# Optimization experiments

Hardware: AMD Instinct MI355X
Metric: run time of the kernel (lower is better)

Reference implementation:

```python
import jax, jax.numpy as jnp
import numpy as np

N, E, EMB, HID, H = 50000, 800000, 128, 512, 8
D = EMB // H
EPS = 1e-5


def _linear_params(key, fan_in, fan_out):
    s = 1.0 / np.sqrt(fan_in)
    k1, k2 = jax.random.split(key)
    w = jax.random.uniform(k1, (fan_in, fan_out), minval=-s, maxval=s, dtype=jnp.float32)
    b = jax.random.uniform(k2, (fan_out,), minval=-s, maxval=s, dtype=jnp.float32)
    return w, b


def setup_inputs() -> dict:
    key = jax.random.key(0)
    ks = jax.random.split(key, 9)
    x = jax.random.normal(ks[0], (N, EMB), dtype=jnp.float32)
    edge_index = jax.random.randint(ks[1], (2, E), 0, N, dtype=jnp.int32)
    batch = jnp.zeros((N,), dtype=jnp.int32)
    wq, bq = _linear_params(ks[2], EMB, EMB)
    wk, bk = _linear_params(ks[3], EMB, EMB)
    wv, bv = _linear_params(ks[4], EMB, EMB)
    wo, bo = _linear_params(ks[5], EMB, EMB)
    w1, b1 = _linear_params(ks[6], EMB, HID)
    w2, b2 = _linear_params(ks[7], HID, EMB)
    g1 = jnp.ones((EMB,), jnp.float32); be1 = jnp.zeros((EMB,), jnp.float32)
    g2 = jnp.ones((EMB,), jnp.float32); be2 = jnp.zeros((EMB,), jnp.float32)
    return {"x": x, "wq": wq, "bq": bq, "wk": wk, "bk": bk, "wv": wv, "bv": bv,
            "wo": wo, "bo": bo, "w1": w1, "b1": b1, "w2": w2, "b2": b2,
            "g1": g1, "be1": be1, "g2": g2, "be2": be2,
            "edge_index": edge_index, "batch": batch, "latent": 0}


def _batchnorm(x, g, b):
    mu = x.mean(axis=0)
    var = ((x - mu) ** 2).mean(axis=0)  # biased, as BatchNorm1d in training
    return g * (x - mu) * jax.lax.rsqrt(var + EPS) + b


def _forward(x, wq, bq, wk, bk, wv, bv, wo, bo, w1, b1, w2, b2, g1, be1, g2, be2, A, B):
    n = x.shape[0]
    q = (x @ wq + bq).reshape(n, H, D)
    k = (x @ wk + bk).reshape(n, H, D)
    v = (x @ wv + bv).reshape(n, H, D)
    # per-edge head-mixing scores: q[A] @ k[B]^T -> [E, H, H]
    score = jnp.einsum('ehd,egd->ehg', q[A], k[B])
    ssum = jax.ops.segment_sum(score, A, num_segments=n)
    cnt = jax.ops.segment_sum(jnp.ones((A.shape[0],), score.dtype), A, num_segments=n)
    score = ssum / jnp.maximum(cnt, 1.0)[:, None, None]  # scatter-mean per node [N,H,H]
    score = jax.nn.softmax(score, axis=-1)
    out = jnp.einsum('ehg,egd->ehd', score, v).reshape(n, EMB)
    out = out @ wo + bo
    x = _batchnorm(out + x, g1, be1)
    h = jax.nn.gelu(x @ w1 + b1, approximate=False)
    h = h @ w2 + b2
    x = _batchnorm(h + x, g2, be2)
    return x


def reference(x, wq, bq, wk, bk, wv, bv, wo, bo, w1, b1, w2, b2, g1, be1, g2, be2, edge_index, batch, latent):
    A, B = edge_index[0], edge_index[1]
    return _forward(x, wq, bq, wk, bk, wv, bv, wo, bo, w1, b1, w2, b2, g1, be1, g2, be2, A, B)
```

## Files before the change

### kernel.cpp

```cpp
#include <hip/hip_runtime.h>
#include <hip/hip_bf16.h>

typedef float f4 __attribute__((ext_vector_type(4)));
typedef short bh8 __attribute__((ext_vector_type(8)));

#define EMB 128
#define HID 512

__device__ __forceinline__ float bfbits2f(unsigned int lo16) {
    unsigned int u = lo16 << 16;
    return __builtin_bit_cast(float, u);
}
__device__ __forceinline__ short f2bf(float f) {
    __hip_bfloat16 h = __float2bfloat16(f);
    return __builtin_bit_cast(short, h);
}

__global__ void hist_kernel(const int* __restrict__ edge, unsigned* __restrict__ cnt, int E) {
    int stride = gridDim.x * blockDim.x;
    for (int e = blockIdx.x * blockDim.x + threadIdx.x; e < E; e += stride)
        atomicAdd(&cnt[edge[e]], 1u);
}

__global__ void scan_blocks(const unsigned* __restrict__ cnt, int* __restrict__ off,
                            int* __restrict__ bsum, int n) {
    __shared__ int ls[256];
    int tid = threadIdx.x;
    int base = blockIdx.x * 1024 + tid * 4;
    int v0 = 0, v1 = 0, v2 = 0, v3 = 0;
    if (base + 0 < n) v0 = (int)cnt[base + 0];
    if (base + 1 < n) v1 = (int)cnt[base + 1];
    if (base + 2 < n) v2 = (int)cnt[base + 2];
    if (base + 3 < n) v3 = (int)cnt[base + 3];
    int s = v0 + v1 + v2 + v3;
    ls[tid] = s;
    __syncthreads();
    for (int d = 1; d < 256; d <<= 1) {
        int t = (tid >= d) ? ls[tid - d] : 0;
        __syncthreads();
        ls[tid] += t;
        __syncthreads();
    }
    int incl = ls[tid];
    int run = incl - s;
    if (tid == 255) bsum[blockIdx.x] = incl;
    if (base + 0 < n) { off[base + 0] = run; run += v0; }
    if (base + 1 < n) { off[base + 1] = run; run += v1; }
    if (base + 2 < n) { off[base + 2] = run; run += v2; }
    if (base + 3 < n) { off[base + 3] = run; }
}

__global__ void scan_bsums(int* __restrict__ bsum, int nb) {
    int lane = threadIdx.x & 63;
    int x = (lane < nb) ? bsum[lane] : 0;
    int orig = x;
#pragma unroll
    for (int o = 1; o < 64; o <<= 1) {
        int t = __shfl_up(x, o, 64);
        if (lane >= o) x += t;
    }
    if (lane < nb) bsum[lane] = x - orig;
}

__global__ void scan_apply(const unsigned* __restrict__ cnt, const int* __restrict__ bsum,
                           int* __restrict__ off, int* __restrict__ offw,
                           float* __restrict__ cntf, int n) {
    int base = blockIdx.x * 1024 + threadIdx.x * 4;
    int add = bsum[blockIdx.x];
#pragma unroll
    for (int i = 0; i < 4; ++i) {
        int idx = base + i;
        if (idx < n) {
            int o = off[idx] + add;
            off[idx] = o;
            offw[idx] = o;
            cntf[idx] = (float)cnt[idx];
        }
    }
}

__global__ void place_kernel(const int* __restrict__ edge, int* __restrict__ offw,
                             int* __restrict__ sortedB, int E) {
    int stride = gridDim.x * blockDim.x;
    for (int e = blockIdx.x * blockDim.x + threadIdx.x; e < E; e += stride) {
        int a = edge[e];
        int pos = atomicAdd(&offw[a], 1);
        sortedB[pos] = edge[E + e];
    }
}

__global__ void prep_all(const float* __restrict__ wq, const float* __restrict__ wk,
                         const float* __restrict__ wv, const float* __restrict__ wo,
                         const float* __restrict__ w1, const float* __restrict__ w2,
                         const float* __restrict__ bq, const float* __restrict__ bk,
                         const float* __restrict__ bv,
                         short* __restrict__ wqkvT, short* __restrict__ woT,
                         short* __restrict__ w1T, short* __restrict__ w2T,
                         float* __restrict__ bqkv) {
    int id = blockIdx.x * blockDim.x + threadIdx.x;
    if (id < 16384) {
        int k = id >> 7, c = id & 127;
        wqkvT[c * 128 + k] = f2bf(wq[id]);
    } else if (id < 32768) {
        int t = id - 16384; int k = t >> 7, c = t & 127;
        wqkvT[(128 + c) * 128 + k] = f2bf(wk[t]);
    } else if (id < 49152) {
        int t = id - 32768; int k = t >> 7, c = t & 127;
        wqkvT[(256 + c) * 128 + k] = f2bf(wv[t]);
    } else if (id < 65536) {
        int t = id - 49152; int k = t >> 7, c = t & 127;
        woT[c * 128 + k] = f2bf(wo[t]);
    } else if (id < 131072) {
        int t = id - 65536; int k = t >> 9, c = t & 511;
        w1T[c * 128 + k] = f2bf(w1[t]);
    } else if (id < 196608) {
        int t = id - 131072; int k = t >> 7, c = t & 127;
        w2T[c * 512 + k] = f2bf(w2[t]);
    }
    if (id < 128) {
        bqkv[id] = bq[id];
        bqkv[128 + id] = bk[id];
        bqkv[256 + id] = bv[id];
    }
}

template<int KT, bool IN_BF16>
__device__ __forceinline__ void ld_ab(bh8 (&av)[4], bh8 (&bv)[4],
                                      const float* __restrict__ Xf, const short* __restrict__ Xb,
                                      const int (&rowA)[4], const short* __restrict__ Wt,
                                      int C0, int l15, int kbase) {
#pragma unroll
    for (int rf = 0; rf < 4; ++rf) {
        if constexpr (IN_BF16) {
            av[rf] = *(const bh8*)(Xb + (size_t)rowA[rf] * KT + kbase);
        } else {
            f4 lo = *(const f4*)(Xf + (size_t)rowA[rf] * KT + kbase);
            f4 hi = *(const f4*)(Xf + (size_t)rowA[rf] * KT + kbase + 4);
            bh8 t;
            t[0] = f2bf(lo[0]); t[1] = f2bf(lo[1]); t[2] = f2bf(lo[2]); t[3] = f2bf(lo[3]);
            t[4] = f2bf(hi[0]); t[5] = f2bf(hi[1]); t[6] = f2bf(hi[2]); t[7] = f2bf(hi[3]);
            av[rf] = t;
        }
    }
#pragma unroll
    for (int cf = 0; cf < 4; ++cf)
        bv[cf] = *(const bh8*)(Wt + (size_t)(C0 + cf * 16 + l15) * KT + kbase);
}

__device__ __forceinline__ void mm16(f4 (&acc)[4][4], const bh8 (&av)[4], const bh8 (&bv)[4]) {
#pragma unroll
    for (int rf = 0; rf < 4; ++rf)
#pragma unroll
        for (int cf = 0; cf < 4; ++cf)
            acc[rf][cf] = __builtin_amdgcn_mfma_f32_16x16x32_bf16(av[rf], bv[cf], acc[rf][cf], 0, 0, 0);
}

#define CSTRIDE 136

template<int KT, bool IN_BF16, bool GELU, bool OUT_BF16, bool RESID, bool RBF16, bool STATS>
__global__ __launch_bounds__(256, 2) void mfma_gemm(
    const void* __restrict__ Xv, const short* __restrict__ Wt, const float* __restrict__ bias,
    const void* __restrict__ resid,
    void* __restrict__ outv, float* __restrict__ slots, int n, int OC, int ncolb, int nrb)
{
    int bx, by;
    if (ncolb == 1) {
        bx = blockIdx.x; by = 0;
    } else {
        int q = blockIdx.x >> 3;
        by = q % ncolb;
        bx = (q / ncolb) * 8 + (blockIdx.x & 7);
        if (bx >= nrb) return;
    }
    const int lane = threadIdx.x & 63;
    const int w = threadIdx.x >> 6;
    const int wr = w >> 1, wc = w & 1;
    const int R0 = bx * 128 + wr * 64;
    const int C0 = by * 128 + wc * 64;
    const int l15 = lane & 15;
    const int kg = lane >> 4;

    const float* Xf = (const float*)Xv;
    const short* Xb = (const short*)Xv;

    int rowA[4];
#pragma unroll
    for (int rf = 0; rf < 4; ++rf) rowA[rf] = min(R0 + rf * 16 + l15, n - 1);

    f4 acc[4][4];
#pragma unroll
    for (int rf = 0; rf < 4; ++rf)
#pragma unroll
        for (int cf = 0; cf < 4; ++cf) acc[rf][cf] = 0.f;

    constexpr int NT = KT / 32;
    bh8 aA[4], bA[4], aB[4], bB[4];

    ld_ab<KT, IN_BF16>(aA, bA, Xf, Xb, rowA, Wt, C0, l15, kg * 8);
#pragma unroll
    for (int t = 0; t < NT; t += 2) {
        ld_ab<KT, IN_BF16>(aB, bB, Xf, Xb, rowA, Wt, C0, l15, (t + 1) * 32 + kg * 8);
        mm16(acc, aA, bA);
        if (t + 2 < NT)
            ld_ab<KT, IN_BF16>(aA, bA, Xf, Xb, rowA, Wt, C0, l15, (t + 2) * 32 + kg * 8);
        mm16(acc, aB, bB);
    }

    if constexpr (OUT_BF16) {
        extern __shared__ short cs[];
        const int lrb = wr * 64;
        const int lcb = wc * 64;
#pragma unroll
        for (int cf = 0; cf < 4; ++cf) {
            const float bcol = bias[C0 + cf * 16 + l15];
#pragma unroll
            for (int rf = 0; rf < 4; ++rf) {
#pragma unroll
                for (int i = 0; i < 4; ++i) {
                    float val = acc[rf][cf][i] + bcol;
                    if constexpr (GELU) val = 0.5f * val * (1.0f + erff(val * 0.70710678f));
                    cs[(lrb + rf * 16 + kg * 4 + i) * CSTRIDE + lcb + cf * 16 + l15] = f2bf(val);
                }
            }
        }
        __syncthreads();
        const int tc = threadIdx.x & 15;
        const int tr = threadIdx.x >> 4;
        const int gcb = by * 128;
#pragma unroll
        for (int r = 0; r < 8; ++r) {
            int lrow = tr + r * 16;
            int grow = bx * 128 + lrow;
            if (grow < n) {
                bh8 v = *(bh8*)(cs + lrow * CSTRIDE + tc * 8);
                *(bh8*)((short*)outv + (size_t)grow * OC + gcb + tc * 8) = v;
            }
        }
    } else {
#pragma unroll
        for (int cf = 0; cf < 4; ++cf) {
            const int col = C0 + cf * 16 + l15;
            const float bcol = bias[col];
#pragma unroll
            for (int rf = 0; rf < 4; ++rf) {
                float s = 0.f, q = 0.f;
#pragma unroll
                for (int i = 0; i < 4; ++i) {
                    const int row = R0 + rf * 16 + kg * 4 + i;
                    if (row < n) {
                        float val = acc[rf][cf][i] + bcol;
                        if constexpr (RESID) {
                            float rv;
                            if constexpr (RBF16)
                                rv = bfbits2f((unsigned short)((const short*)resid)[(size_t)row * EMB + col]);
                            else
                                rv = ((const float*)resid)[(size_t)row * EMB + col];
                            val += rv;
                        }
                        if constexpr (GELU) val = 0.5f * val * (1.0f + erff(val * 0.70710678f));
                        if constexpr (STATS) { s += val; q += val * val; }
                        ((float*)outv)[(size_t)row * OC + col] = val;
                    }
                }
                if constexpr (STATS) {
                    s += __shfl_xor(s, 16, 64); s += __shfl_xor(s, 32, 64);
                    q += __shfl_xor(q, 16, 64); q += __shfl_xor(q, 32, 64);
                    if (kg == 0) {
                        float* sl = slots + (size_t)(bx & 63) * 256;
                        unsafeAtomicAdd(&sl[col], s);
                        unsafeAtomicAdd(&sl[128 + col], q);
                    }
                }
            }
        }
    }
}

__global__ void gather_attn_kernel(const short* __restrict__ qkv, const int* __restrict__ off,
                                   const unsigned* __restrict__ cnt, const int* __restrict__ sortedB,
                                   const float* __restrict__ cntf, short* __restrict__ attno, int n) {
    int wid = (int)((blockIdx.x * blockDim.x + threadIdx.x) >> 6);
    int lane = threadIdx.x & 63;
    int nw = (gridDim.x * blockDim.x) >> 6;
    const int l15 = lane & 15;
    const int grp = lane >> 4;
    const int h = lane >> 3, g = lane & 7;
    for (int node = wid; node < n; node += nw) {
        int start = off[node];
        int deg = (int)cnt[node];
        float a[8];
#pragma unroll
        for (int i = 0; i < 8; ++i) a[i] = 0.f;
        for (int j = 0; j < deg; j += 8) {
            int i0 = j + grp, i1 = j + 4 + grp;
            uint4 u0 = make_uint4(0, 0, 0, 0), u1 = make_uint4(0, 0, 0, 0);
            if (i0 < deg) {
                int b = sortedB[start + i0];
                u0 = *(const uint4*)(qkv + (size_t)b * 384 + 128 + l15 * 8);
            }
            if (i1 < deg) {
                int b = sortedB[start + i1];
                u1 = *(const uint4*)(qkv + (size_t)b * 384 + 128 + l15 * 8);
            }
            unsigned w0[4] = {u0.x, u0.y, u0.z, u0.w};
            unsigned w1[4] = {u1.x, u1.y, u1.z, u1.w};
#pragma unroll
            for (int i = 0; i < 4; ++i) {
                a[2 * i]     += bfbits2f(w0[i] & 0xffffu) + bfbits2f(w1[i] & 0xffffu);
                a[2 * i + 1] += bfbits2f(w0[i] >> 16)     + bfbits2f(w1[i] >> 16);
            }
        }
#pragma unroll
        for (int i = 0; i < 8; ++i) {
            a[i] += __shfl_xor(a[i], 16, 64);
            a[i] += __shfl_xor(a[i], 32, 64);
        }

        const short* qp = qkv + (size_t)node * 384 + h * 16;
        uint4 qa = *(const uint4*)qp;
        uint4 qb = *(const uint4*)(qp + 8);
        float qv[16];
        {
            unsigned ua[4] = {qa.x, qa.y, qa.z, qa.w};
            unsigned ub[4] = {qb.x, qb.y, qb.z, qb.w};
#pragma unroll
            for (int w2 = 0; w2 < 4; ++w2) {
                qv[2 * w2]         = bfbits2f(ua[w2] & 0xffffu);
                qv[2 * w2 + 1]     = bfbits2f(ua[w2] >> 16);
                qv[8 + 2 * w2]     = bfbits2f(ub[w2] & 0xffffu);
                qv[8 + 2 * w2 + 1] = bfbits2f(ub[w2] >> 16);
            }
        }
        float s = 0.f;
#pragma unroll
        for (int i = 0; i < 8; ++i) {
            s += qv[i]     * __shfl(a[i], 2 * g, 64);
            s += qv[8 + i] * __shfl(a[i], 2 * g + 1, 64);
        }
        float c = cntf[node];
        s *= 1.0f / fmaxf(c, 1.0f);
        float m = s;
#pragma unroll
        for (int o = 1; o < 8; o <<= 1) m = fmaxf(m, __shfl_xor(m, o, 64));
        float e = __expf(s - m);
        float sum = e;
#pragma unroll
        for (int o = 1; o < 8; o <<= 1) sum += __shfl_xor(sum, o, 64);
        float p = e / sum;
        float o0 = 0.f, o1 = 0.f;
        int d0 = g * 2;
#pragma unroll
        for (int gg = 0; gg < 8; ++gg) {
            float pg = __shfl(p, h * 8 + gg, 64);
            unsigned vv = *(const unsigned*)(qkv + (size_t)node * 384 + 256 + gg * 16 + d0);
            o0 += pg * bfbits2f(vv & 0xffffu);
            o1 += pg * bfbits2f(vv >> 16);
        }
        unsigned pk = (unsigned)(unsigned short)f2bf(o0) | ((unsigned)(unsigned short)f2bf(o1) << 16);
        *(unsigned*)(attno + (size_t)node * EMB + h * 16 + d0) = pk;
    }
}

__global__ void bn_finalize_slots(const float* __restrict__ slots, float* __restrict__ scsh,
                                  const float* __restrict__ g, const float* __restrict__ be, int n) {
    int c = threadIdx.x;
    float s = 0.f, q = 0.f;
    for (int i = 0; i < 64; ++i) {
        s += slots[(size_t)i * 256 + c];
        q += slots[(size_t)i * 256 + 128 + c];
    }
    float invn = 1.0f / (float)n;
    float mean = s * invn;
    float var = fmaxf(q * invn - mean * mean, 0.f);
    float sc = g[c] * rsqrtf(var + 1e-5f);
    scsh[c] = sc;
    scsh[128 + c] = be[c] - mean * sc;
}

__global__ void apply_bn_bf16(const float* __restrict__ Y, const float* __restrict__ scsh,
                              short* __restrict__ out, size_t total8) {
    size_t stride = (size_t)gridDim.x * blockDim.x;
    for (size_t i = (size_t)blockIdx.x * blockDim.x + threadIdx.x; i < total8; i += stride) {
        size_t base = i * 8;
        f4 lo = *(const f4*)(Y + base);
        f4 hi = *(const f4*)(Y + base + 4);
        int c = (int)(base & 127);
        f4 s0 = *(const f4*)(scsh + c);
        f4 s1 = *(const f4*)(scsh + c + 4);
        f4 h0 = *(const f4*)(scsh + 128 + c);
        f4 h1 = *(const f4*)(scsh + 128 + c + 4);
        lo = lo * s0 + h0;
        hi = hi * s1 + h1;
        bh8 o;
        o[0] = f2bf(lo[0]); o[1] = f2bf(lo[1]); o[2] = f2bf(lo[2]); o[3] = f2bf(lo[3]);
        o[4] = f2bf(hi[0]); o[5] = f2bf(hi[1]); o[6] = f2bf(hi[2]); o[7] = f2bf(hi[3]);
        *(bh8*)(out + base) = o;
    }
}

__global__ void bn_apply(float* __restrict__ Y, const float* __restrict__ scsh, size_t total4) {
    size_t stride = (size_t)gridDim.x * blockDim.x;
    for (size_t i = (size_t)blockIdx.x * blockDim.x + threadIdx.x; i < total4; i += stride) {
        f4 vv = ((f4*)Y)[i];
        int c = (int)((i * 4) & 127);
#pragma unroll
        for (int j = 0; j < 4; ++j) vv[j] = vv[j] * scsh[c + j] + scsh[128 + c + j];
        ((f4*)Y)[i] = vv;
    }
}

extern "C" void kernel_launch(void* const* d_in, const int* in_sizes, int n_in,
                              void* d_out, int out_size, void* d_ws, size_t ws_size,
                              hipStream_t stream) {
    const float* x   = (const float*)d_in[0];
    const float* wq  = (const float*)d_in[1];
    const float* bq  = (const float*)d_in[2];
    const float* wk  = (const float*)d_in[3];
    const float* bk  = (const float*)d_in[4];
    const float* wv  = (const float*)d_in[5];
    const float* bv  = (const float*)d_in[6];
    const float* wo  = (const float*)d_in[7];
    const float* bo  = (const float*)d_in[8];
    const float* w1  = (const float*)d_in[9];
    const float* b1  = (const float*)d_in[10];
    const float* w2  = (const float*)d_in[11];
    const float* b2  = (const float*)d_in[12];
    const float* g1  = (const float*)d_in[13];
    const float* be1 = (const float*)d_in[14];
    const float* g2  = (const float*)d_in[15];
    const float* be2 = (const float*)d_in[16];
    const int* edge  = (const int*)d_in[17];

    int n = in_sizes[0] / EMB;
    int E = in_sizes[17] / 2;

    float* wsf = (float*)d_ws;
    unsigned* cnt_u = (unsigned*)wsf;
    float*  cntf  = wsf + 65536;
    int*    off   = (int*)(wsf + 2 * 65536);
    int*    offw  = (int*)(wsf + 3 * 65536);
    int*    bsum  = (int*)(wsf + 4 * 65536);
    int*    sortedB = (int*)(wsf + 4 * 65536 + 64);
    float*  base5 = wsf + 4 * 65536 + 64 + E;
    short*  qkv   = (short*)base5;
    short*  ksum  = (short*)(base5 + (size_t)n * 192);
    short*  attno = (short*)(base5 + (size_t)n * 256);
    float*  y1    = base5 + (size_t)n * 320;
    float*  warea = y1 + (size_t)n * 128;
    short*  wqkvT = (short*)warea;
    short*  woT   = wqkvT + 384 * 128;
    short*  w1T   = woT + 128 * 128;
    short*  w2T   = w1T + 512 * 128;
    float*  bqkv  = (float*)(w2T + 128 * 512);
    float*  slots1 = bqkv + 384;
    float*  slots2 = slots1 + 64 * 256;
    float*  scsh1  = slots2 + 64 * 256;
    float*  scsh2  = scsh1 + 256;
    short*  hbuf  = qkv;
    short*  xn1   = attno;
    float*  y2    = (float*)d_out;
    (void)ksum;

    hipMemsetAsync(cnt_u, 0, 65536 * sizeof(unsigned), stream);
    hipMemsetAsync(slots1, 0, 2 * 64 * 256 * sizeof(float), stream);

    int nb = (n + 1023) / 1024;
    hist_kernel<<<2048, 256, 0, stream>>>(edge, cnt_u, E);
    scan_blocks<<<nb, 256, 0, stream>>>(cnt_u, off, bsum, n);
    scan_bsums<<<1, 64, 0, stream>>>(bsum, nb);
    scan_apply<<<nb, 256, 0, stream>>>(cnt_u, bsum, off, offw, cntf, n);
    place_kernel<<<2048, 256, 0, stream>>>(edge, offw, sortedB, E);

    prep_all<<<768, 256, 0, stream>>>(wq, wk, wv, wo, w1, w2, bq, bk, bv,
                                      wqkvT, woT, w1T, w2T, bqkv);

    int nrb = (n + 127) / 128;
    int nrb8 = ((nrb + 7) / 8) * 8;
    const size_t CSH = 128 * CSTRIDE * sizeof(short);

    mfma_gemm<128, false, false, true, false, false, false><<<nrb8 * 3, 256, CSH, stream>>>(
        x, wqkvT, bqkv, nullptr, qkv, nullptr, n, 384, 3, nrb);

    gather_attn_kernel<<<2048, 256, 0, stream>>>(qkv, off, cnt_u, sortedB, cntf, attno, n);

    mfma_gemm<128, true, false, false, true, false, true><<<nrb, 256, 0, stream>>>(
        attno, woT, bo, x, y1, slots1, n, EMB, 1, nrb);

    bn_finalize_slots<<<1, 128, 0, stream>>>(slots1, scsh1, g1, be1, n);

    apply_bn_bf16<<<1600, 256, 0, stream>>>(y1, scsh1, xn1, (size_t)n * EMB / 8);

    mfma_gemm<128, true, true, true, false, false, false><<<nrb8 * 4, 256, CSH, stream>>>(
        xn1, w1T, b1, nullptr, hbuf, nullptr, n, HID, 4, nrb);

    mfma_gemm<512, true, false, false, true, true, true><<<nrb, 256, 0, stream>>>(
        hbuf, w2T, b2, xn1, y2, slots2, n, EMB, 1, nrb);

    bn_finalize_slots<<<1, 128, 0, stream>>>(slots2, scsh2, g2, be2, n);
    bn_apply<<<512, 256, 0, stream>>>(y2, scsh2, (size_t)n * EMB / 4);
}
```

Measured before the change: 335.2 us.

## Fuse FFN up-projection, GELU and down-projection into one kernel

Replaces the two FFN GEMM launches with a single kernel that computes each 128-column chunk of the hidden layer, applies bias and exact GELU, stages it as bf16 in shared memory, and immediately accumulates it into the down-projection. This avoids writing and re-reading the N×512 bf16 hidden buffer through global memory and saves one launch. The cost is a grid of only nrb blocks (about 391) with serialized chunk loops and direct global loads of A/B fragments, so parallelism per kernel is lower and there is extra synchronisation.

```diff
diff --git a/kernel.cpp b/kernel.cpp
--- a/kernel.cpp
+++ b/kernel.cpp
@@ -276,6 +276,114 @@
     }
 }
 
+__global__ __launch_bounds__(256, 2) void ffn_fused(
+    const short* __restrict__ xn1, const short* __restrict__ w1T, const float* __restrict__ b1,
+    const short* __restrict__ w2T, const float* __restrict__ b2,
+    float* __restrict__ y2, float* __restrict__ slots, int n)
+{
+    extern __shared__ short hs[];
+    const int bx = blockIdx.x;
+    const int lane = threadIdx.x & 63;
+    const int w = threadIdx.x >> 6;
+    const int wr = w >> 1, wc = w & 1;
+    const int R0 = bx * 128 + wr * 64;
+    const int l15 = lane & 15;
+    const int kg = lane >> 4;
+
+    int rowA[4];
+#pragma unroll
+    for (int rf = 0; rf < 4; ++rf) rowA[rf] = min(R0 + rf * 16 + l15, n - 1);
+
+    f4 acc2[4][4];
+#pragma unroll
+    for (int rf = 0; rf < 4; ++rf)
+#pragma unroll
+        for (int cf = 0; cf < 4; ++cf) acc2[rf][cf] = 0.f;
+
+    for (int c = 0; c < 4; ++c) {
+        f4 acc1[4][4];
+#pragma unroll
+        for (int rf = 0; rf < 4; ++rf)
+#pragma unroll
+            for (int cf = 0; cf < 4; ++cf) acc1[rf][cf] = 0.f;
+#pragma unroll
+        for (int ks = 0; ks < 4; ++ks) {
+            const int kbase = ks * 32 + kg * 8;
+            bh8 a1[4], b1f[4];
+#pragma unroll
+            for (int rf = 0; rf < 4; ++rf)
+                a1[rf] = *(const bh8*)(xn1 + (size_t)rowA[rf] * EMB + kbase);
+#pragma unroll
+            for (int cf = 0; cf < 4; ++cf) {
+                int col = c * 128 + wc * 64 + cf * 16 + l15;
+                b1f[cf] = *(const bh8*)(w1T + (size_t)col * EMB + kbase);
+            }
+            mm16(acc1, a1, b1f);
+        }
+        __syncthreads();
+        {
+            const int lrb = wr * 64;
+            const int lcb = wc * 64;
+#pragma unroll
+            for (int cf = 0; cf < 4; ++cf) {
+                const float bcol = b1[c * 128 + wc * 64 + cf * 16 + l15];
+#pragma unroll
+                for (int rf = 0; rf < 4; ++rf) {
+#pragma unroll
+                    for (int i = 0; i < 4; ++i) {
+                        float val = acc1[rf][cf][i] + bcol;
+                        val = 0.5f * val * (1.0f + erff(val * 0.70710678f));
+                        hs[(lrb + rf * 16 + kg * 4 + i) * CSTRIDE + lcb + cf * 16 + l15] = f2bf(val);
+                    }
+                }
+            }
+        }
+        __syncthreads();
+#pragma unroll
+        for (int ks = 0; ks < 4; ++ks) {
+            const int kbase = ks * 32 + kg * 8;
+            bh8 a2[4], b2f[4];
+#pragma unroll
+            for (int rf = 0; rf < 4; ++rf)
+                a2[rf] = *(const bh8*)(hs + (wr * 64 + rf * 16 + l15) * CSTRIDE + kbase);
+#pragma unroll
+            for (int cf = 0; cf < 4; ++cf) {
+                int col = wc * 64 + cf * 16 + l15;
+                b2f[cf] = *(const bh8*)(w2T + (size_t)col * HID + c * 128 + kbase);
+            }
+            mm16(acc2, a2, b2f);
+        }
+    }
+
+    const int C0 = wc * 64;
+#pragma unroll
+    for (int cf = 0; cf < 4; ++cf) {
+        const int col = C0 + cf * 16 + l15;
+        const float bcol = b2[col];
+#pragma unroll
+        for (int rf = 0; rf < 4; ++rf) {
+            float s = 0.f, q = 0.f;
+#pragma unroll
+            for (int i = 0; i < 4; ++i) {
+                const int row = R0 + rf * 16 + kg * 4 + i;
+                if (row < n) {
+                    float val = acc2[rf][cf][i] + bcol;
+                    val += bfbits2f((unsigned short)xn1[(size_t)row * EMB + col]);
+                    s += val; q += val * val;
+                    y2[(size_t)row * EMB + col] = val;
+                }
+            }
+            s += __shfl_xor(s, 16, 64); s += __shfl_xor(s, 32, 64);
+            q += __shfl_xor(q, 16, 64); q += __shfl_xor(q, 32, 64);
+            if (kg == 0) {
+                float* sl = slots + (size_t)(bx & 63) * 256;
+                unsafeAtomicAdd(&sl[col], s);
+                unsafeAtomicAdd(&sl[128 + col], q);
+            }
+        }
+    }
+}
+
 __global__ void gather_attn_kernel(const short* __restrict__ qkv, const int* __restrict__ off,
                                    const unsigned* __restrict__ cnt, const int* __restrict__ sortedB,
                                    const float* __restrict__ cntf, short* __restrict__ attno, int n) {
@@ -443,7 +551,6 @@
     int*    sortedB = (int*)(wsf + 4 * 65536 + 64);
     float*  base5 = wsf + 4 * 65536 + 64 + E;
     short*  qkv   = (short*)base5;
-    short*  ksum  = (short*)(base5 + (size_t)n * 192);
     short*  attno = (short*)(base5 + (size_t)n * 256);
     float*  y1    = base5 + (size_t)n * 320;
     float*  warea = y1 + (size_t)n * 128;
@@ -456,10 +563,8 @@
     float*  slots2 = slots1 + 64 * 256;
     float*  scsh1  = slots2 + 64 * 256;
     float*  scsh2  = scsh1 + 256;
-    short*  hbuf  = qkv;
     short*  xn1   = attno;
     float*  y2    = (float*)d_out;
-    (void)ksum;
 
     hipMemsetAsync(cnt_u, 0, 65536 * sizeof(unsigned), stream);
     hipMemsetAsync(slots1, 0, 2 * 64 * 256 * sizeof(float), stream);
@@ -490,11 +595,7 @@
 
     apply_bn_bf16<<<1600, 256, 0, stream>>>(y1, scsh1, xn1, (size_t)n * EMB / 8);
 
-    mfma_gemm<128, true, true, true, false, false, false><<<nrb8 * 4, 256, CSH, stream>>>(
-        xn1, w1T, b1, nullptr, hbuf, nullptr, n, HID, 4, nrb);
-
-    mfma_gemm<512, true, false, false, true, true, true><<<nrb, 256, 0, stream>>>(
-        hbuf, w2T, b2, xn1, y2, slots2, n, EMB, 1, nrb);
+    ffn_fused<<<nrb, 256, CSH, stream>>>(xn1, w1T, b1, w2T, b2, y2, slots2, n);
 
     bn_finalize_slots<<<1, 128, 0, stream>>>(slots2, scsh2, g2, be2, n);
     bn_apply<<<512, 256, 0, stream>>>(y2, scsh2, (size_t)n * EMB / 4);
```

Result: faster. 308.8 us (-7.9%).
